# Performance work log

Measured on AMD Instinct MI355X. Metric: run time of the kernel, lower is better.

Reference implementation:

```python
import math
import jax, jax.numpy as jnp
import numpy as np

B, S, IN_DIM, D_MODEL, L, T_Y = 16, 512, 64, 64, 32, 256
T_X = T_Y + L - 1
RIDGE = 0.01
THRESH = 0.005


def _pos_encoding(seq_len, d):
    pos = jnp.arange(seq_len, dtype=jnp.float32)[:, None]
    div = jnp.exp(jnp.arange(0, d, 2, dtype=jnp.float32) * (-(math.log(10000.0) / d)))
    ang = pos * div  # [S, d/2]
    pe = jnp.zeros((seq_len, d), dtype=jnp.float32)
    pe = pe.at[:, 0::2].set(jnp.sin(ang)).at[:, 1::2].set(jnp.cos(ang))
    return pe


def _layernorm(h, gamma, beta, eps=1e-5):
    mu = jnp.mean(h, axis=-1, keepdims=True)
    var = jnp.mean((h - mu) ** 2, axis=-1, keepdims=True)
    return (h - mu) * jax.lax.rsqrt(var + eps) * gamma + beta


def setup_inputs() -> dict:
    key = jax.random.key(0)
    ks = jax.random.split(key, 8)
    return {
        "fps": jax.random.normal(ks[0], (B, S, IN_DIM), dtype=jnp.float32),
        "x": jax.random.normal(ks[1], (B, S, T_X), dtype=jnp.float32),
        "y": jax.random.normal(ks[2], (B, S, T_Y), dtype=jnp.float32),
        "sample_steps": jax.random.randint(ks[3], (5,), 10, S),
        "W1": jax.random.normal(ks[4], (IN_DIM, 256), dtype=jnp.float32) / math.sqrt(IN_DIM),
        "b1": jnp.zeros((256,), dtype=jnp.float32),
        "gamma": jnp.ones((256,), dtype=jnp.float32),
        "beta": jnp.zeros((256,), dtype=jnp.float32),
        "W2": jax.random.normal(ks[5], (256, D_MODEL), dtype=jnp.float32) / math.sqrt(256.0),
        "b2": jnp.zeros((D_MODEL,), dtype=jnp.float32),
        "Wq": jax.random.normal(ks[6], (D_MODEL, D_MODEL), dtype=jnp.float32) / math.sqrt(D_MODEL),
        "bq": jnp.zeros((D_MODEL,), dtype=jnp.float32),
        "Wk": jax.random.normal(ks[7], (D_MODEL, D_MODEL), dtype=jnp.float32) / math.sqrt(D_MODEL),
        "bk": jnp.zeros((D_MODEL,), dtype=jnp.float32),
    }


def reference(fps, x, y, sample_steps, W1, b1, gamma, beta, W2, b2, Wq, bq, Wk, bk):
    batch, seq_len, _ = fps.shape
    d = Wq.shape[0]
    t_y = y.shape[-1]
    filt = x.shape[-1] - t_y + 1  # L

    # encoder: Linear -> LayerNorm -> Tanh -> Linear -> Tanh
    h = _layernorm(fps @ W1 + b1, gamma, beta)
    e_orig = jnp.tanh(jnp.tanh(h) @ W2 + b2)  # [B,S,d]
    e = e_orig + 0.05 * _pos_encoding(seq_len, d)[None]

    q = e @ Wq + bq
    k = e @ Wk + bk
    scores = jnp.einsum('bsd,btd->bst', q, k) / math.sqrt(d)
    causal = jnp.triu(jnp.ones((seq_len, seq_len), dtype=bool), 1)
    scores = jnp.where(causal[None], -1e9, scores)
    alpha = jax.nn.softmax(scores * 2.0, axis=-1)  # [B,S,S]

    # sliding windows: X[b,s] = unfold(x[b,s], L, 1)[:T_y] -> [T_y, L]
    win = jnp.arange(t_y)[:, None] + jnp.arange(filt)[None, :]
    X = x[:, :, win]  # [B,S,T_y,L]

    # per-source gram / cross contributions
    G = jnp.einsum('bstl,bstm->bslm', X, X)  # [B,S,L,L]
    C = jnp.einsum('bstl,bst->bsl', X, y)    # [B,S,L]

    w = alpha[:, sample_steps, :]            # [B,T,S]
    wm = jnp.where(w > THRESH, w, 0.0)

    gram = jnp.einsum('bts,bslm->btlm', wm, G) + RIDGE * jnp.eye(filt, dtype=x.dtype)
    cross = jnp.einsum('bts,bsl->btl', wm, C)
    wt_hat = jnp.linalg.solve(gram, cross[..., None])[..., 0]  # [B,T,L]

    Xt = X[:, sample_steps]  # [B,T,T_y,L]
    yt = y[:, sample_steps]  # [B,T,T_y]
    pred = jnp.einsum('btkl,btl->btk', Xt, wt_hat)
    loss_bt = jnp.mean((yt - pred) ** 2, axis=-1)  # [B,T]

    valid = jnp.any(wm > 0.0, axis=-1)  # [B,T]
    total = jnp.sum(jnp.where(valid, loss_bt, 0.0))
    n = jnp.maximum(jnp.sum(valid.astype(jnp.int32)), 1)
    loss = total / n
    return loss, alpha, e_orig
```

## Files before the change

kernel.cpp:

```cpp
#include <hip/hip_runtime.h>
#include <hip/hip_bf16.h>
#include <math.h>

#define BB 16
#define SS 512
#define INDIM 64
#define DMODEL 64
#define HID 256
#define FILT 32
#define TYY 256
#define TXX 287
#define NT 5
#define RIDGEF 0.01f
#define THRESHF 0.005f

__global__ __launch_bounds__(256) void k_mlp(
    const float* __restrict__ fps, const float* __restrict__ W1, const float* __restrict__ b1,
    const float* __restrict__ gamma, const float* __restrict__ beta,
    const float* __restrict__ W2, const float* __restrict__ b2,
    const float* __restrict__ Wq, const float* __restrict__ bq,
    const float* __restrict__ Wk, const float* __restrict__ bk,
    float* __restrict__ e_out, float* __restrict__ q_out, float* __restrict__ kT_out)
{
    const int row0 = blockIdx.x << 2;
    const int tid = threadIdx.x;

    __shared__ float fr[4][INDIM];
    __shared__ float red[4][256];
    __shared__ float th4[4][HID];
    __shared__ float ee4[4][DMODEL];
    __shared__ float part4[4][4][DMODEL];
    __shared__ float partk4[4][4][DMODEL];

    { int r = tid >> 6, i = tid & 63;
      fr[r][i] = fps[(row0 + r) * INDIM + i]; }
    __syncthreads();

    float h[4];
    float b1v = b1[tid];
    #pragma unroll
    for (int r = 0; r < 4; ++r) h[r] = b1v;
    for (int i = 0; i < INDIM; ++i) {
        float w = W1[i * HID + tid];
        #pragma unroll
        for (int r = 0; r < 4; ++r) h[r] = fmaf(fr[r][i], w, h[r]);
    }

    #pragma unroll
    for (int r = 0; r < 4; ++r) red[r][tid] = h[r];
    __syncthreads();
    for (int off = 128; off > 0; off >>= 1) {
        if (tid < off) {
            #pragma unroll
            for (int r = 0; r < 4; ++r) red[r][tid] += red[r][tid + off];
        }
        __syncthreads();
    }
    float mu[4];
    #pragma unroll
    for (int r = 0; r < 4; ++r) mu[r] = red[r][0] * (1.0f / HID);
    __syncthreads();
    #pragma unroll
    for (int r = 0; r < 4; ++r) { float d = h[r] - mu[r]; red[r][tid] = d * d; }
    __syncthreads();
    for (int off = 128; off > 0; off >>= 1) {
        if (tid < off) {
            #pragma unroll
            for (int r = 0; r < 4; ++r) red[r][tid] += red[r][tid + off];
        }
        __syncthreads();
    }
    float gm = gamma[tid], bt = beta[tid];
    #pragma unroll
    for (int r = 0; r < 4; ++r) {
        float var = red[r][0] * (1.0f / HID);
        float hn = (h[r] - mu[r]) * rsqrtf(var + 1e-5f) * gm + bt;
        th4[r][tid] = tanhf(hn);
    }
    __syncthreads();

    { int p = tid >> 6, j = tid & 63;
      float acc[4] = {0.f, 0.f, 0.f, 0.f};
      for (int i = p * 64; i < p * 64 + 64; ++i) {
          float w = W2[i * DMODEL + j];
          #pragma unroll
          for (int r = 0; r < 4; ++r) acc[r] = fmaf(th4[r][i], w, acc[r]);
      }
      #pragma unroll
      for (int r = 0; r < 4; ++r) part4[p][r][j] = acc[r];
    }
    __syncthreads();
    { int r = tid >> 6, j = tid & 63;
      float e = part4[0][r][j] + part4[1][r][j] + part4[2][r][j] + part4[3][r][j] + b2[j];
      float eo = tanhf(e);
      int row = row0 + r;
      int s = row & (SS - 1);
      e_out[(size_t)row * DMODEL + j] = eo;
      float div = expf(-(float)(j & ~1) * 0.14391156831212787f);
      float ang = (float)s * div;
      float pe = (j & 1) ? cosf(ang) : sinf(ang);
      ee4[r][j] = eo + 0.05f * pe;
    }
    __syncthreads();
    { int p = tid >> 6, j = tid & 63;
      float aq[4] = {0.f,0.f,0.f,0.f}, ak[4] = {0.f,0.f,0.f,0.f};
      for (int i = p * 16; i < p * 16 + 16; ++i) {
          float wqv = Wq[i * DMODEL + j];
          float wkv = Wk[i * DMODEL + j];
          #pragma unroll
          for (int r = 0; r < 4; ++r) {
              aq[r] = fmaf(ee4[r][i], wqv, aq[r]);
              ak[r] = fmaf(ee4[r][i], wkv, ak[r]);
          }
      }
      #pragma unroll
      for (int r = 0; r < 4; ++r) { part4[p][r][j] = aq[r]; partk4[p][r][j] = ak[r]; }
    }
    __syncthreads();
    { int r = tid >> 6, j = tid & 63;
      float qv = part4[0][r][j] + part4[1][r][j] + part4[2][r][j] + part4[3][r][j] + bq[j];
      float kv = partk4[0][r][j] + partk4[1][r][j] + partk4[2][r][j] + partk4[3][r][j] + bk[j];
      int row = row0 + r;
      int b = row >> 9, s = row & (SS - 1);
      q_out[(size_t)row * DMODEL + j] = qv;
      kT_out[(size_t)(b * DMODEL + j) * SS + s] = kv;
    }
}

__global__ __launch_bounds__(256) void k_attn(
    const float* __restrict__ q, const float* __restrict__ kT,
    float* __restrict__ alpha)
{
    const int blk = blockIdx.x;
    const int b = blk >> 7;
    const int t0 = (blk & 127) << 2;
    const int t3 = t0 + 3;
    const int tid = threadIdx.x;
    const int wave = tid >> 6, lane = tid & 63;

    __shared__ float qt[4 * DMODEL];
    __shared__ float redm[4][4];

    qt[tid] = q[(size_t)(b * SS + t0 + (tid >> 6)) * DMODEL + (tid & 63)];
    __syncthreads();

    const float* kTb = kT + (size_t)b * DMODEL * SS;
    const int s0 = tid, s1 = tid + 256;
    float a0[4] = {0,0,0,0}, a1[4] = {0,0,0,0};
    if (s1 <= t3) {
        for (int d = 0; d < DMODEL; ++d) {
            float k0 = kTb[d * SS + s0];
            float k1 = kTb[d * SS + s1];
            #pragma unroll
            for (int r = 0; r < 4; ++r) {
                float qv = qt[r * DMODEL + d];
                a0[r] = fmaf(qv, k0, a0[r]);
                a1[r] = fmaf(qv, k1, a1[r]);
            }
        }
    } else if (s0 <= t3) {
        for (int d = 0; d < DMODEL; ++d) {
            float k0 = kTb[d * SS + s0];
            #pragma unroll
            for (int r = 0; r < 4; ++r) a0[r] = fmaf(qt[r * DMODEL + d], k0, a0[r]);
        }
    }
    float lg0[4], lg1[4];
    #pragma unroll
    for (int r = 0; r < 4; ++r) {
        int tr = t0 + r;
        lg0[r] = (s0 <= tr) ? 0.25f * a0[r] : -INFINITY;
        lg1[r] = (s1 <= tr) ? 0.25f * a1[r] : -INFINITY;
    }
    float mr[4];
    #pragma unroll
    for (int r = 0; r < 4; ++r) {
        float m = fmaxf(lg0[r], lg1[r]);
        #pragma unroll
        for (int off = 32; off > 0; off >>= 1) m = fmaxf(m, __shfl_xor(m, off));
        if (lane == 0) redm[r][wave] = m;
    }
    __syncthreads();
    #pragma unroll
    for (int r = 0; r < 4; ++r)
        mr[r] = fmaxf(fmaxf(redm[r][0], redm[r][1]), fmaxf(redm[r][2], redm[r][3]));
    __syncthreads();
    float ex0[4], ex1[4], sr[4];
    #pragma unroll
    for (int r = 0; r < 4; ++r) {
        ex0[r] = expf(lg0[r] - mr[r]);
        ex1[r] = expf(lg1[r] - mr[r]);
        float sm = ex0[r] + ex1[r];
        #pragma unroll
        for (int off = 32; off > 0; off >>= 1) sm += __shfl_xor(sm, off);
        if (lane == 0) redm[r][wave] = sm;
    }
    __syncthreads();
    #pragma unroll
    for (int r = 0; r < 4; ++r)
        sr[r] = redm[r][0] + redm[r][1] + redm[r][2] + redm[r][3];
    #pragma unroll
    for (int r = 0; r < 4; ++r) {
        float inv = 1.0f / sr[r];
        size_t base = (size_t)(b * SS + t0 + r) * SS;
        alpha[base + s0] = ex0[r] * inv;
        alpha[base + s1] = ex1[r] * inv;
    }
}

__global__ __launch_bounds__(256) void k_gpart(
    const float* __restrict__ x, const float* __restrict__ y,
    const int* __restrict__ steps, const float* __restrict__ alpha,
    float* __restrict__ part, int C, int CS)
{
    const int b = blockIdx.x / C;
    const int chunk = blockIdx.x % C;
    const int tid = threadIdx.x;
    const int lane = tid & 63, wid = tid >> 6;

    __shared__ float xs[288];
    __shared__ float ys[256];
    __shared__ float Gs[1056];
    __shared__ float crossL[32];
    __shared__ float wv[NT * 64];
    __shared__ int sl[64];
    __shared__ int nselS;
    __shared__ int stS[NT];
    __shared__ float redA[4][33];
    __shared__ float redB[4][33];

    if (tid < NT) stS[tid] = steps[tid];
    if (tid < 32) Gs[tid * 33 + 32] = 0.f;
    __syncthreads();

    for (int idx = tid; idx < NT * CS; idx += 256) {
        int t = idx / CS, si = idx % CS;
        float a = alpha[(size_t)(b * SS + stS[t]) * SS + chunk * CS + si];
        wv[t * 64 + si] = (a > THRESHF) ? a : 0.f;
    }
    __syncthreads();
    if (tid == 0) {
        int c = 0;
        for (int si = 0; si < CS; ++si) {
            float m = wv[si] + wv[64 + si] + wv[128 + si] + wv[192 + si] + wv[256 + si];
            if (m > 0.f) sl[c++] = si;
        }
        nselS = c;
    }
    __syncthreads();
    const int nsel = nselS;

    float acc[NT][5];
    #pragma unroll
    for (int t = 0; t < NT; ++t) {
        #pragma unroll
        for (int r = 0; r < 5; ++r) acc[t][r] = 0.f;
    }

    float rx0 = 0.f, rx1 = 0.f, ry = 0.f;
    if (nsel > 0) {
        int sg = chunk * CS + sl[0];
        const float* xr = x + (size_t)(b * SS + sg) * TXX;
        const float* yr = y + (size_t)(b * SS + sg) * TYY;
        rx0 = xr[tid];
        if (tid < 31) rx1 = xr[256 + tid];
        ry = yr[tid];
    }

    for (int i = 0; i < nsel; ++i) {
        xs[tid] = rx0;
        if (tid < 31) xs[256 + tid] = rx1;
        ys[tid] = ry;
        const int sl_cur = sl[i];
        __syncthreads();

        if (i + 1 < nsel) {
            int sg = chunk * CS + sl[i + 1];
            const float* xr = x + (size_t)(b * SS + sg) * TXX;
            const float* yr = y + (size_t)(b * SS + sg) * TYY;
            rx0 = xr[tid];
            if (tid < 31) rx1 = xr[256 + tid];
            ry = yr[tid];
        }

        { int l = tid & 31, p = tid >> 5;
          float c = 0.f, a = 0.f;
          const int k0 = p * 32;
          #pragma unroll
          for (int kk = 0; kk < 32; ++kk) {
              int k = k0 + kk;
              float xv = xs[k + l];
              c = fmaf(xv, ys[k], c);
              a = fmaf(xs[k], xv, a);
          }
          c += __shfl_xor(c, 32);
          a += __shfl_xor(a, 32);
          if (lane < 32) { redA[wid][l] = c; redB[wid][l] = a; }
        }
        __syncthreads();

        if (tid < 32)
            crossL[tid] = redA[0][tid] + redA[1][tid] + redA[2][tid] + redA[3][tid];

        { int jj = lane & 31;
          #pragma unroll
          for (int pass = 0; pass < 4; ++pass) {
              int dd = 2 * (wid + 4 * pass) + (lane >> 5);
              float g0 = redB[0][dd] + redB[1][dd] + redB[2][dd] + redB[3][dd];
              float dlt = 0.f;
              if (jj > 0 && jj + dd < 32)
                  dlt = xs[jj + 255] * xs[jj + 255 + dd]
                      - xs[jj - 1] * xs[jj - 1 + dd];
              #pragma unroll
              for (int off = 1; off < 32; off <<= 1) {
                  float tsh = __shfl_up(dlt, off, 32);
                  if (jj >= off) dlt += tsh;
              }
              if (jj + dd < 32) {
                  float gval = g0 + dlt;
                  Gs[jj * 33 + jj + dd] = gval;
                  Gs[(jj + dd) * 33 + jj] = gval;
              }
          }
        }
        __syncthreads();

        #pragma unroll
        for (int t = 0; t < NT; ++t) {
            float w = wv[t * 64 + sl_cur];
            if (w > 0.f) {
                #pragma unroll
                for (int r = 0; r < 4; ++r)
                    acc[t][r] = fmaf(w, Gs[tid + 256 * r], acc[t][r]);
                if (tid < 32)      acc[t][4] = fmaf(w, Gs[1024 + tid], acc[t][4]);
                else if (tid < 64) acc[t][4] = fmaf(w, crossL[tid - 32], acc[t][4]);
            }
        }
    }

    #pragma unroll
    for (int t = 0; t < NT; ++t) {
        size_t base = (size_t)((b * NT + t) * C + chunk) * 1088;
        #pragma unroll
        for (int r = 0; r < 4; ++r) part[base + tid + 256 * r] = acc[t][r];
        if (tid < 64) part[base + 1024 + tid] = acc[t][4];
    }
}

__global__ __launch_bounds__(256) void k_solve2(
    const float* __restrict__ x, const float* __restrict__ y,
    const int* __restrict__ steps, const float* __restrict__ alpha,
    const float* __restrict__ part,
    float* __restrict__ lossbt, int* __restrict__ valid, int C)
{
    const int g = blockIdx.x;
    const int b = g / NT, t = g % NT;
    const int tid = threadIdx.x;

    __shared__ float Af[1056];
    __shared__ float zs[FILT];
    __shared__ float wt[FILT];
    __shared__ float xsr[TXX + 1];
    __shared__ float red[256];
    __shared__ int step_s;
    __shared__ int anyv;

    if (tid == 0) { step_s = steps[t]; anyv = 0; }
    __syncthreads();

    float a0 = 0.f, a1 = 0.f, a2 = 0.f, a3 = 0.f, a4 = 0.f;
    for (int ch = 0; ch < C; ++ch) {
        const float* pp = part + (size_t)(g * C + ch) * 1088;
        a0 += pp[tid];
        a1 += pp[tid + 256];
        a2 += pp[tid + 512];
        a3 += pp[tid + 768];
        if (tid < 64) a4 += pp[tid + 1024];
    }
    Af[tid] = a0; Af[tid + 256] = a1; Af[tid + 512] = a2; Af[tid + 768] = a3;
    if (tid < 32) Af[1024 + tid] = a4;
    else if (tid < 64) zs[tid - 32] = a4;

    { const float* arow = alpha + (size_t)(b * SS + step_s) * SS;
      if (arow[tid] > THRESHF || arow[tid + 256] > THRESHF) anyv = 1; }
    __syncthreads();
    if (tid < 32) Af[tid * 33 + tid] += RIDGEF;
    __syncthreads();

    for (int k = 0; k < FILT; ++k) {
        if (tid < FILT && tid >= k) {
            float dk = sqrtf(Af[k * 33 + k]);
            if (tid == k) Af[k * 33 + k] = dk;
            else          Af[tid * 33 + k] = Af[tid * 33 + k] / dk;
        }
        __syncthreads();
        #pragma unroll
        for (int r = 0; r < 4; ++r) {
            int idx = tid + 256 * r, i = idx >> 5, j = idx & 31;
            if (i > k && j > k && j <= i)
                Af[i * 33 + j] -= Af[i * 33 + k] * Af[j * 33 + k];
        }
        __syncthreads();
    }

    if (tid < 64) {
        int l = tid & 31;
        float zl = zs[l];
        for (int k = 0; k < FILT; ++k) {
            float lkk = Af[k * 33 + k];
            float zk = __shfl(zl, k, 64) / lkk;
            if (l == k) zl = zk;
            else if (l > k) zl = fmaf(-Af[l * 33 + k], zk, zl);
        }
        for (int k = FILT - 1; k >= 0; --k) {
            float lkk = Af[k * 33 + k];
            float zk = __shfl(zl, k, 64) / lkk;
            if (l == k) zl = zk;
            else if (l < k) zl = fmaf(-Af[k * 33 + l], zk, zl);
        }
        if (tid < 32) wt[l] = zl;
    }
    __syncthreads();

    const int sstep = step_s;
    const float* xrow = x + (size_t)(b * SS + sstep) * TXX;
    for (int i = tid; i < TXX; i += 256) xsr[i] = xrow[i];
    __syncthreads();
    float pk = 0.f;
    #pragma unroll
    for (int l = 0; l < FILT; ++l) pk = fmaf(xsr[tid + l], wt[l], pk);
    float d = y[(size_t)(b * SS + sstep) * TYY + tid] - pk;
    red[tid] = d * d;
    __syncthreads();
    for (int off = 128; off > 0; off >>= 1) {
        if (tid < off) red[tid] += red[tid + off];
        __syncthreads();
    }
    if (tid == 0) {
        lossbt[g] = red[0] * (1.0f / TYY);
        valid[g] = anyv;
    }
}

__global__ __launch_bounds__(128) void k_final(
    const float* __restrict__ lossbt, const int* __restrict__ valid,
    float* __restrict__ out0)
{
    __shared__ float rs[128];
    __shared__ int rc[128];
    int tid = threadIdx.x;
    float v = 0.f; int c = 0;
    if (tid < BB * NT && valid[tid]) { v = lossbt[tid]; c = 1; }
    rs[tid] = v; rc[tid] = c;
    __syncthreads();
    for (int off = 64; off > 0; off >>= 1) {
        if (tid < off) { rs[tid] += rs[tid + off]; rc[tid] += rc[tid + off]; }
        __syncthreads();
    }
    if (tid == 0) {
        int n = rc[0] > 0 ? rc[0] : 1;
        out0[0] = rs[0] / (float)n;
    }
}

extern "C" void kernel_launch(void* const* d_in, const int* in_sizes, int n_in,
                              void* d_out, int out_size, void* d_ws, size_t ws_size,
                              hipStream_t stream)
{
    const float* fps  = (const float*)d_in[0];
    const float* x    = (const float*)d_in[1];
    const float* y    = (const float*)d_in[2];
    const int* steps  = (const int*)d_in[3];
    const float* W1   = (const float*)d_in[4];
    const float* b1   = (const float*)d_in[5];
    const float* gamma= (const float*)d_in[6];
    const float* beta = (const float*)d_in[7];
    const float* W2   = (const float*)d_in[8];
    const float* b2   = (const float*)d_in[9];
    const float* Wq   = (const float*)d_in[10];
    const float* bq   = (const float*)d_in[11];
    const float* Wk   = (const float*)d_in[12];
    const float* bk   = (const float*)d_in[13];

    float* out   = (float*)d_out;
    float* alpha = out + 1;
    float* e_out = out + 1 + (size_t)BB * SS * SS;

    float* lossbt = (float*)d_ws;
    int*   valid  = (int*)(lossbt + 128);
    float* shreg  = (float*)d_ws + 256;
    float* q      = shreg;
    float* kT     = q + (size_t)BB * SS * DMODEL;
    float* part   = shreg;

    size_t avail_f = (ws_size > 1024) ? (ws_size / 4 - 256) : 0;
    int C = 32;
    while (C > 8 && (size_t)(BB * NT) * C * 1088 > avail_f) C >>= 1;
    int CS = SS / C;

    hipLaunchKernelGGL(k_mlp, dim3(BB * SS / 4), dim3(256), 0, stream,
                       fps, W1, b1, gamma, beta, W2, b2, Wq, bq, Wk, bk,
                       e_out, q, kT);
    hipLaunchKernelGGL(k_attn, dim3(BB * (SS / 4)), dim3(256), 0, stream,
                       q, kT, alpha);
    hipLaunchKernelGGL(k_gpart, dim3(BB * C), dim3(256), 0, stream,
                       x, y, steps, alpha, part, C, CS);
    hipLaunchKernelGGL(k_solve2, dim3(BB * NT), dim3(256), 0, stream,
                       x, y, steps, alpha, part, lossbt, valid, C);
    hipLaunchKernelGGL(k_final, dim3(1), dim3(128), 0, stream, lossbt, valid, out);
}
```

Baseline: 213.8 us.

## Use wave-shuffle reductions, register Cholesky, vectorized LDS reads, more chunks

Replaces the shared-memory tree reductions in the LayerNorm with wave shuffles and a one-pass sum/sum-of-squares variance. Rewrites the 32x32 Cholesky and triangular solves in k_solve2 to run in registers within one wave, removing per-column block barriers. Vectorizes LDS reads in the gram inner loop, hoists G loads out of the per-step loop, and doubles the number of chunks in k_gpart. The one-pass variance can lose precision, and the extra chunks add partial-sum traffic.

```diff
diff --git a/kernel.cpp b/kernel.cpp
--- a/kernel.cpp
+++ b/kernel.cpp
@@ -24,13 +24,14 @@
 {
     const int row0 = blockIdx.x << 2;
     const int tid = threadIdx.x;
+    const int wid = tid >> 6, lane = tid & 63;
 
     __shared__ float fr[4][INDIM];
-    __shared__ float red[4][256];
     __shared__ float th4[4][HID];
     __shared__ float ee4[4][DMODEL];
     __shared__ float part4[4][4][DMODEL];
     __shared__ float partk4[4][4][DMODEL];
+    __shared__ float wred[4][4][2];
 
     { int r = tid >> 6, i = tid & 63;
       fr[r][i] = fps[(row0 + r) * INDIM + i]; }
@@ -46,35 +47,30 @@
         for (int r = 0; r < 4; ++r) h[r] = fmaf(fr[r][i], w, h[r]);
     }
 
-    #pragma unroll
-    for (int r = 0; r < 4; ++r) red[r][tid] = h[r];
-    __syncthreads();
-    for (int off = 128; off > 0; off >>= 1) {
-        if (tid < off) {
-            #pragma unroll
-            for (int r = 0; r < 4; ++r) red[r][tid] += red[r][tid + off];
-        }
-        __syncthreads();
-    }
-    float mu[4];
-    #pragma unroll
-    for (int r = 0; r < 4; ++r) mu[r] = red[r][0] * (1.0f / HID);
-    __syncthreads();
-    #pragma unroll
-    for (int r = 0; r < 4; ++r) { float d = h[r] - mu[r]; red[r][tid] = d * d; }
-    __syncthreads();
-    for (int off = 128; off > 0; off >>= 1) {
-        if (tid < off) {
-            #pragma unroll
-            for (int r = 0; r < 4; ++r) red[r][tid] += red[r][tid + off];
-        }
-        __syncthreads();
-    }
+    float s1[4], s2[4];
+    #pragma unroll
+    for (int r = 0; r < 4; ++r) { s1[r] = h[r]; s2[r] = h[r] * h[r]; }
+    #pragma unroll
+    for (int off = 1; off < 64; off <<= 1) {
+        #pragma unroll
+        for (int r = 0; r < 4; ++r) {
+            s1[r] += __shfl_xor(s1[r], off);
+            s2[r] += __shfl_xor(s2[r], off);
+        }
+    }
+    if (lane == 0) {
+        #pragma unroll
+        for (int r = 0; r < 4; ++r) { wred[wid][r][0] = s1[r]; wred[wid][r][1] = s2[r]; }
+    }
+    __syncthreads();
     float gm = gamma[tid], bt = beta[tid];
     #pragma unroll
     for (int r = 0; r < 4; ++r) {
-        float var = red[r][0] * (1.0f / HID);
-        float hn = (h[r] - mu[r]) * rsqrtf(var + 1e-5f) * gm + bt;
+        float t1 = wred[0][r][0] + wred[1][r][0] + wred[2][r][0] + wred[3][r][0];
+        float t2 = wred[0][r][1] + wred[1][r][1] + wred[2][r][1] + wred[3][r][1];
+        float mu = t1 * (1.0f / HID);
+        float var = t2 * (1.0f / HID) - mu * mu;
+        float hn = (h[r] - mu) * rsqrtf(var + 1e-5f) * gm + bt;
         th4[r][tid] = tanhf(hn);
     }
     __syncthreads();
@@ -218,8 +214,8 @@
     const int tid = threadIdx.x;
     const int lane = tid & 63, wid = tid >> 6;
 
-    __shared__ float xs[288];
-    __shared__ float ys[256];
+    __shared__ __align__(16) float xs[288];
+    __shared__ __align__(16) float ys[256];
     __shared__ float Gs[1056];
     __shared__ float crossL[32];
     __shared__ float wv[NT * 64];
@@ -284,14 +280,20 @@
         }
 
         { int l = tid & 31, p = tid >> 5;
+          const float4* xk4 = (const float4*)(xs + (p << 5));
+          const float4* yk4 = (const float4*)(ys + (p << 5));
           float c = 0.f, a = 0.f;
-          const int k0 = p * 32;
           #pragma unroll
-          for (int kk = 0; kk < 32; ++kk) {
-              int k = k0 + kk;
-              float xv = xs[k + l];
-              c = fmaf(xv, ys[k], c);
-              a = fmaf(xs[k], xv, a);
+          for (int j = 0; j < 8; ++j) {
+              float4 xk = xk4[j];
+              float4 yk = yk4[j];
+              int kb = (p << 5) + (j << 2);
+              float x0 = xs[kb + l],     x1 = xs[kb + 1 + l];
+              float x2 = xs[kb + 2 + l], x3 = xs[kb + 3 + l];
+              c = fmaf(x0, yk.x, c); a = fmaf(xk.x, x0, a);
+              c = fmaf(x1, yk.y, c); a = fmaf(xk.y, x1, a);
+              c = fmaf(x2, yk.z, c); a = fmaf(xk.z, x2, a);
+              c = fmaf(x3, yk.w, c); a = fmaf(xk.w, x3, a);
           }
           c += __shfl_xor(c, 32);
           a += __shfl_xor(a, 32);
@@ -325,16 +327,20 @@
         }
         __syncthreads();
 
-        #pragma unroll
-        for (int t = 0; t < NT; ++t) {
-            float w = wv[t * 64 + sl_cur];
-            if (w > 0.f) {
-                #pragma unroll
-                for (int r = 0; r < 4; ++r)
-                    acc[t][r] = fmaf(w, Gs[tid + 256 * r], acc[t][r]);
-                if (tid < 32)      acc[t][4] = fmaf(w, Gs[1024 + tid], acc[t][4]);
-                else if (tid < 64) acc[t][4] = fmaf(w, crossL[tid - 32], acc[t][4]);
-            }
+        { float g0 = Gs[tid], g1 = Gs[tid + 256], g2 = Gs[tid + 512], g3 = Gs[tid + 768];
+          float g4 = (tid < 32) ? Gs[1024 + tid]
+                   : ((tid < 64) ? crossL[tid - 32] : 0.f);
+          #pragma unroll
+          for (int t = 0; t < NT; ++t) {
+              float w = wv[t * 64 + sl_cur];
+              if (w > 0.f) {
+                  acc[t][0] = fmaf(w, g0, acc[t][0]);
+                  acc[t][1] = fmaf(w, g1, acc[t][1]);
+                  acc[t][2] = fmaf(w, g2, acc[t][2]);
+                  acc[t][3] = fmaf(w, g3, acc[t][3]);
+                  acc[t][4] = fmaf(w, g4, acc[t][4]);
+              }
+          }
         }
     }
 
@@ -387,38 +393,42 @@
     if (tid < 32) Af[tid * 33 + tid] += RIDGEF;
     __syncthreads();
 
-    for (int k = 0; k < FILT; ++k) {
-        if (tid < FILT && tid >= k) {
-            float dk = sqrtf(Af[k * 33 + k]);
-            if (tid == k) Af[k * 33 + k] = dk;
-            else          Af[tid * 33 + k] = Af[tid * 33 + k] / dk;
-        }
-        __syncthreads();
-        #pragma unroll
-        for (int r = 0; r < 4; ++r) {
-            int idx = tid + 256 * r, i = idx >> 5, j = idx & 31;
-            if (i > k && j > k && j <= i)
-                Af[i * 33 + j] -= Af[i * 33 + k] * Af[j * 33 + k];
-        }
-        __syncthreads();
-    }
-
-    if (tid < 64) {
-        int l = tid & 31;
-        float zl = zs[l];
-        for (int k = 0; k < FILT; ++k) {
-            float lkk = Af[k * 33 + k];
-            float zk = __shfl(zl, k, 64) / lkk;
-            if (l == k) zl = zk;
-            else if (l > k) zl = fmaf(-Af[l * 33 + k], zk, zl);
-        }
-        for (int k = FILT - 1; k >= 0; --k) {
-            float lkk = Af[k * 33 + k];
-            float zk = __shfl(zl, k, 64) / lkk;
-            if (l == k) zl = zk;
-            else if (l < k) zl = fmaf(-Af[k * 33 + l], zk, zl);
-        }
-        if (tid < 32) wt[l] = zl;
+    if (tid < 32) {
+        float a[32];
+        #pragma unroll
+        for (int j = 0; j < 32; ++j) a[j] = Af[tid * 33 + j];
+        #pragma unroll
+        for (int k = 0; k < 32; ++k) {
+            float akk = __shfl(a[k], k);
+            float dk = sqrtf(akk);
+            float ck = a[k] / dk;
+            if (tid >= k) a[k] = ck;
+            #pragma unroll
+            for (int m = k + 1; m < 32; ++m) {
+                float cm = __shfl(ck, m);
+                if (tid >= m) a[m] = fmaf(-ck, cm, a[m]);
+            }
+        }
+        #pragma unroll
+        for (int j = 0; j < 32; ++j)
+            if (j <= tid) Af[tid * 33 + j] = a[j];
+
+        float zl = zs[tid];
+        #pragma unroll
+        for (int k = 0; k < 32; ++k) {
+            float akk = __shfl(a[k], k);
+            float zk = __shfl(zl, k) / akk;
+            if (tid == k) zl = zk;
+            else if (tid > k) zl = fmaf(-a[k], zk, zl);
+        }
+        #pragma unroll
+        for (int k = 31; k >= 0; --k) {
+            float akk = __shfl(a[k], k);
+            float wk = __shfl(zl, k) / akk;
+            if (tid == k) zl = wk;
+            else if (tid < k) zl = fmaf(-Af[k * 33 + tid], wk, zl);
+        }
+        wt[tid] = zl;
     }
     __syncthreads();
 
@@ -494,7 +504,7 @@
     float* part   = shreg;
 
     size_t avail_f = (ws_size > 1024) ? (ws_size / 4 - 256) : 0;
-    int C = 32;
+    int C = 64;
     while (C > 8 && (size_t)(BB * NT) * C * 1088 > avail_f) C >>= 1;
     int CS = SS / C;
 
```

Measured after the change: 209.9 us. About the same (-1.8%).
